# Kernel tuning notes

Hardware: AMD Instinct MI355X
Metric: run time of the kernel (lower is better)

The kernel has to match this reference:

```python
import jax, jax.numpy as jnp
import numpy as np

H = 16      # num_heads
EPS = 1e-6  # LayerNorm eps


def _ln(x, g, b):
    m = jnp.mean(x, -1, keepdims=True)
    v = jnp.mean((x - m) ** 2, -1, keepdims=True)
    return (x - m) / jnp.sqrt(v + EPS) * g + b


def _mha(q_in, k_in, v_in, qw, qb, kw, kb, vw, vb, pw, pb, mask):
    # q_in: (B, Sq, C); k_in/v_in: (B, Skv, C); mask: bool (Sq, Skv) or None (True = masked)
    B, Sq, C = q_in.shape
    hd = C // H

    def split(x, w, bb):
        return (x @ w + bb).reshape(B, -1, H, hd).transpose(0, 2, 1, 3)  # (B,H,S,hd)

    q = split(q_in, qw, qb) * hd ** -0.5
    k = split(k_in, kw, kb)
    v = split(v_in, vw, vb)
    s = jnp.einsum('bhqd,bhkd->bhqk', q, k)  # (B,H,Sq,Skv)
    if mask is not None:
        s = jnp.where(mask, -jnp.inf, s)
    a = jax.nn.softmax(s, axis=-1)
    o = jnp.einsum('bhqk,bhkd->bhqd', a, v)
    return o.transpose(0, 2, 1, 3).reshape(B, Sq, C) @ pw + pb


def _mlp(x, w1, b1, w2, b2):
    # torch nn.GELU default is exact (erf) gelu
    return jax.nn.gelu(x @ w1 + b1, approximate=False) @ w2 + b2


def setup_inputs() -> dict:
    key = jax.random.key(0)
    B, S, C, M = 1, 2048, 1024, 4096
    ks = iter(jax.random.split(key, 64))

    def w(shape):
        return jax.random.normal(next(ks), shape, jnp.float32) * 0.02

    inp = {
        'features': jax.random.normal(next(ks), (B, S, C), jnp.float32),
        'encoder_output': jax.random.normal(next(ks), (B, S, C), jnp.float32),
    }
    for p in ['ln1a', 'ln1b', 'ln2a', 'ln2b']:
        inp[p + '_g'] = jnp.ones((C,), jnp.float32)
        inp[p + '_b'] = jnp.zeros((C,), jnp.float32)
    for p in ['sa', 'ca']:
        for q in ['q', 'k', 'v', 'p']:
            inp[f'{p}_{q}w'] = w((C, C))
            inp[f'{p}_{q}b'] = jnp.zeros((C,), jnp.float32)
    for p in ['m1', 'm2']:
        inp[p + '_w1'] = w((C, M))
        inp[p + '_b1'] = jnp.zeros((M,), jnp.float32)
        inp[p + '_w2'] = w((M, C))
        inp[p + '_b2'] = jnp.zeros((C,), jnp.float32)
    return inp


def reference(features, encoder_output,
              ln1a_g, ln1a_b, ln1b_g, ln1b_b, ln2a_g, ln2a_b, ln2b_g, ln2b_b,
              sa_qw, sa_qb, sa_kw, sa_kb, sa_vw, sa_vb, sa_pw, sa_pb,
              ca_qw, ca_qb, ca_kw, ca_kb, ca_vw, ca_vb, ca_pw, ca_pb,
              m1_w1, m1_b1, m1_w2, m1_b2, m2_w1, m2_b1, m2_w2, m2_b2):
    S = features.shape[1]
    causal = jnp.triu(jnp.ones((S, S), dtype=bool), 1)  # look-ahead mask (decoder)
    # self-attention block (pre-norm, residual; dropout/drop-path identity in eval)
    xn = _ln(features, ln1a_g, ln1a_b)
    x = features + _mha(xn, xn, xn, sa_qw, sa_qb, sa_kw, sa_kb, sa_vw, sa_vb, sa_pw, sa_pb, causal)
    x = x + _mlp(_ln(x, ln1b_g, ln1b_b), m1_w1, m1_b1, m1_w2, m1_b2)
    # cross-attention block: k = v = encoder_output, q = norm(x)
    xn = _ln(x, ln2a_g, ln2a_b)
    x = x + _mha(xn, encoder_output, encoder_output, ca_qw, ca_qb, ca_kw, ca_kb, ca_vw, ca_vb, ca_pw, ca_pb, None)
    return x + _mlp(_ln(x, ln2b_g, ln2b_b), m2_w1, m2_b1, m2_w2, m2_b2)
```

## Files before the change

kernel.cpp:

```cpp
#include <hip/hip_runtime.h>
#include <math.h>

typedef unsigned short u16;
typedef __bf16 bf16_t;
typedef bf16_t bf16x8 __attribute__((ext_vector_type(8)));
typedef float f32x4 __attribute__((ext_vector_type(4)));
typedef float f32x16 __attribute__((ext_vector_type(16)));

#define DI __device__ __forceinline__

DI u16 f2bf(float f) {
  union { float f; unsigned u; } c; c.f = f;
  unsigned r = c.u + 0x7FFFu + ((c.u >> 16) & 1u);
  return (u16)(r >> 16);
}

DI unsigned pack2(float lo, float hi_) {
  return (unsigned)f2bf(lo) | ((unsigned)f2bf(hi_) << 16);
}

DI unsigned cvt_pk(float lo, float hi_) {
  unsigned d;
  asm("v_cvt_pk_bf16_f32 %0, %1, %2" : "=v"(d) : "v"(lo), "v"(hi_));
  return d;
}

typedef __attribute__((address_space(1))) void* gas_ptr;
typedef __attribute__((address_space(3))) void* las_ptr;

DI void gload16(const void* g, void* l) {
  __builtin_amdgcn_global_load_lds((gas_ptr)g, (las_ptr)l, 16, 0, 0);
}

struct TransArgs { const float* src[12]; u16* dst[12]; };
__global__ __launch_bounds__(256) void k_transpose_all(TransArgs ta) {
  __shared__ float tile[32][33];
  int bx = blockIdx.x;
  int z, local, K, N;
  if (bx < 8192) { z = bx >> 10; local = bx & 1023; K = 1024; N = 1024; }
  else {
    int i = bx - 8192; z = 8 + (i >> 12); local = i & 4095;
    if (z & 1) { K = 4096; N = 1024; } else { K = 1024; N = 4096; }
  }
  const float* w = ta.src[z];
  u16* wt = ta.dst[z];
  int nT = N >> 5;
  int n0 = (local % nT) * 32, k0 = (local / nT) * 32;
  int tx = threadIdx.x & 31, ty = threadIdx.x >> 5;
  for (int r = ty; r < 32; r += 8)
    tile[r][tx] = w[(size_t)(k0 + r) * N + n0 + tx];
  __syncthreads();
  for (int r = ty; r < 32; r += 8)
    wt[(size_t)(n0 + r) * K + k0 + tx] = f2bf(tile[tx][r]);
}

__global__ __launch_bounds__(256) void k_cvt(const float* __restrict__ in, u16* __restrict__ out, int n4) {
  int i = blockIdx.x * 256 + threadIdx.x;
  if (i < n4) {
    float4 v = ((const float4*)in)[i];
    ushort4 o;
    o.x = f2bf(v.x); o.y = f2bf(v.y); o.z = f2bf(v.z); o.w = f2bf(v.w);
    ((ushort4*)out)[i] = o;
  }
}

__global__ __launch_bounds__(256) void k_biaspack(float* __restrict__ bq, float* __restrict__ bc,
                                                  const float* qb, const float* kb, const float* vb,
                                                  const float* ckb, const float* cvb) {
  int i = blockIdx.x * 256 + threadIdx.x;
  if (i < 1024) bq[i] = qb[i];
  else if (i < 2048) bq[i] = kb[i - 1024];
  else if (i < 3072) bq[i] = vb[i - 2048];
  else if (i < 4096) bc[i - 3072] = ckb[i - 3072];
  else if (i < 5120) bc[i - 3072] = cvb[i - 4096];
}

__global__ __launch_bounds__(256) void k_ln(const float* __restrict__ x, const float* __restrict__ g,
                                            const float* __restrict__ b, u16* __restrict__ out) {
  int row = blockIdx.x, t = threadIdx.x;
  const float4 v = ((const float4*)(x + (size_t)row * 1024))[t];
  float s = v.x + v.y + v.z + v.w;
  float ss = v.x * v.x + v.y * v.y + v.z * v.z + v.w * v.w;
  for (int o = 32; o; o >>= 1) { s += __shfl_down(s, o); ss += __shfl_down(ss, o); }
  __shared__ float red[10];
  int w = t >> 6;
  if ((t & 63) == 0) { red[w] = s; red[4 + w] = ss; }
  __syncthreads();
  if (t == 0) {
    float S = red[0] + red[1] + red[2] + red[3];
    float SS = red[4] + red[5] + red[6] + red[7];
    float mean = S * (1.f / 1024.f);
    float var = SS * (1.f / 1024.f) - mean * mean;
    red[8] = mean; red[9] = rsqrtf(var + 1e-6f);
  }
  __syncthreads();
  float mean = red[8], rstd = red[9];
  float4 gg = ((const float4*)g)[t], bb = ((const float4*)b)[t];
  ushort4 o4;
  o4.x = f2bf((v.x - mean) * rstd * gg.x + bb.x);
  o4.y = f2bf((v.y - mean) * rstd * gg.y + bb.y);
  o4.z = f2bf((v.z - mean) * rstd * gg.z + bb.z);
  o4.w = f2bf((v.w - mean) * rstd * gg.w + bb.w);
  ((ushort4*)(out + (size_t)row * 1024))[t] = o4;
}

template <int MODE>
__global__ __launch_bounds__(256) void k_gemm(const u16* __restrict__ A, const u16* __restrict__ Bt,
                                              const float* __restrict__ bias, void* outv, u16* vtout,
                                              int M, int N, int K, int ostride,
                                              float scale, int scale_end, int vcol0) {
  constexpr int BM = 64, NT = 2;
  __shared__ u16 aL[2][BM * 64];
  __shared__ u16 bL[2][128 * 64];
  const int lane = threadIdx.x & 63, w = threadIdx.x >> 6, t = threadIdx.x;
  const int wn = w;
  const int m0 = blockIdx.y * BM, n0 = blockIdx.x * 128;

  f32x4 acc[4][NT];
#pragma unroll
  for (int i = 0; i < 4; ++i)
#pragma unroll
    for (int j = 0; j < NT; ++j) acc[i][j] = (f32x4){0.f, 0.f, 0.f, 0.f};

  auto stage = [&](int buf, int kt) {
    const int k0 = kt << 6;
#pragma unroll
    for (int c = t; c < BM * 8; c += 256) {
      int row = c >> 3, c16 = c & 7;
      int sw = (c16 * 16) ^ ((row & 7) << 4);
      gload16((const char*)(A + (size_t)(m0 + row) * K + k0) + sw, (char*)aL[buf] + c * 16);
    }
#pragma unroll
    for (int c = t; c < 1024; c += 256) {
      int row = c >> 3, c16 = c & 7;
      int sw = (c16 * 16) ^ ((row & 7) << 4);
      gload16((const char*)(Bt + (size_t)(n0 + row) * K + k0) + sw, (char*)bL[buf] + c * 16);
    }
  };

  const int nkt = K >> 6;
  stage(0, 0);
  __syncthreads();
  int cur = 0;
  for (int kt = 0; kt < nkt; ++kt) {
    if (kt + 1 < nkt) stage(cur ^ 1, kt + 1);
#pragma unroll
    for (int kk = 0; kk < 2; ++kk) {
      const int cb = kk * 64 + ((lane >> 4) << 4);
      bf16x8 af[4], bfr[NT];
#pragma unroll
      for (int mi = 0; mi < 4; ++mi) {
        int row = mi * 16 + (lane & 15);
        af[mi] = *(const bf16x8*)((const char*)aL[cur] + row * 128 + (cb ^ ((row & 7) << 4)));
      }
#pragma unroll
      for (int ni = 0; ni < NT; ++ni) {
        int row = wn * 32 + ni * 16 + (lane & 15);
        bfr[ni] = *(const bf16x8*)((const char*)bL[cur] + row * 128 + (cb ^ ((row & 7) << 4)));
      }
#pragma unroll
      for (int mi = 0; mi < 4; ++mi)
#pragma unroll
        for (int ni = 0; ni < NT; ++ni)
          acc[mi][ni] = __builtin_amdgcn_mfma_f32_16x16x32_bf16(af[mi], bfr[ni], acc[mi][ni], 0, 0, 0);
    }
    __syncthreads();
    cur ^= 1;
  }

  const int cBase = n0 + wn * 32 + (lane & 15);
  const int rBase = m0 + ((lane >> 4) << 2);
#pragma unroll
  for (int ni = 0; ni < NT; ++ni) {
    int col = cBase + ni * 16;
    float bv = bias[col];
#pragma unroll
    for (int mi = 0; mi < 4; ++mi) {
      int row = rBase + mi * 16;
      f32x4 a = acc[mi][ni];
      if (MODE == 0) {
        float sc = (col < scale_end) ? scale : 1.f;
        if (col >= vcol0) {
          ushort4 o4;
          o4.x = f2bf((a[0] + bv) * sc); o4.y = f2bf((a[1] + bv) * sc);
          o4.z = f2bf((a[2] + bv) * sc); o4.w = f2bf((a[3] + bv) * sc);
          *(ushort4*)(vtout + (size_t)(col - vcol0) * M + row) = o4;
        } else {
#pragma unroll
          for (int r = 0; r < 4; ++r)
            ((u16*)outv)[(size_t)(row + r) * ostride + col] = f2bf((a[r] + bv) * sc);
        }
      } else {
#pragma unroll
        for (int r = 0; r < 4; ++r) {
          float v = a[r] + bv;
          ((u16*)outv)[(size_t)(row + r) * ostride + col] =
              f2bf(0.5f * v * (1.f + erff(v * 0.70710678118654752f)));
        }
      }
    }
  }
}

template <int MODE>
__global__ __launch_bounds__(512, 2) void k_gemm_sk(const u16* __restrict__ A, const u16* __restrict__ Bt,
                                                    const float* __restrict__ bias, const float* res,
                                                    void* outv, int M, int N, int K, float scale) {
  __shared__ u16 aL[2][2][64 * 64];
  __shared__ u16 bL[2][2][64 * 64];
  const int t = threadIdx.x, lane = t & 63, w = t >> 6;
  const int kh = w >> 2, ws2 = w & 3;
  const int ts = t & 255;
  const int m0 = blockIdx.y * 64, n0 = blockIdx.x * 64;
  const int nktH = (K >> 6) >> 1;
  const int kbase = kh * nktH;

  f32x4 acc[4];
#pragma unroll
  for (int i = 0; i < 4; ++i) acc[i] = (f32x4){0.f, 0.f, 0.f, 0.f};

  auto stage = [&](int buf, int kt) {
    const int k0 = (kbase + kt) << 6;
#pragma unroll
    for (int i = 0; i < 2; ++i) {
      int c = i * 256 + ts;
      int row = c >> 3, c16 = c & 7;
      int sw = (c16 * 16) ^ ((row & 7) << 4);
      gload16((const char*)(A + (size_t)(m0 + row) * K + k0) + sw, (char*)aL[kh][buf] + c * 16);
      gload16((const char*)(Bt + (size_t)(n0 + row) * K + k0) + sw, (char*)bL[kh][buf] + c * 16);
    }
  };

  stage(0, 0);
  __syncthreads();
  int cur = 0;
  for (int kt = 0; kt < nktH; ++kt) {
    if (kt + 1 < nktH) stage(cur ^ 1, kt + 1);
#pragma unroll
    for (int kk = 0; kk < 2; ++kk) {
      const int cb = kk * 64 + ((lane >> 4) << 4);
      bf16x8 af[4], bfr;
#pragma unroll
      for (int mi = 0; mi < 4; ++mi) {
        int row = mi * 16 + (lane & 15);
        af[mi] = *(const bf16x8*)((const char*)aL[kh][cur] + row * 128 + (cb ^ ((row & 7) << 4)));
      }
      {
        int row = ws2 * 16 + (lane & 15);
        bfr = *(const bf16x8*)((const char*)bL[kh][cur] + row * 128 + (cb ^ ((row & 7) << 4)));
      }
#pragma unroll
      for (int mi = 0; mi < 4; ++mi)
        acc[mi] = __builtin_amdgcn_mfma_f32_16x16x32_bf16(af[mi], bfr, acc[mi], 0, 0, 0);
    }
    __syncthreads();
    cur ^= 1;
  }

  float* mergeF = (float*)aL;
  const int r0l = (lane >> 4) << 2, col16 = lane & 15;
  if (kh == 1) {
#pragma unroll
    for (int mi = 0; mi < 4; ++mi)
#pragma unroll
      for (int r = 0; r < 4; ++r)
        mergeF[(ws2 * 64 + mi * 16 + r0l + r) * 17 + col16] = acc[mi][r];
  }
  __syncthreads();
  if (kh == 0) {
    int col = n0 + ws2 * 16 + col16;
    float bv = bias[col];
#pragma unroll
    for (int mi = 0; mi < 4; ++mi) {
      int row = m0 + mi * 16 + r0l;
#pragma unroll
      for (int r = 0; r < 4; ++r) {
        float v = acc[mi][r] + mergeF[(ws2 * 64 + mi * 16 + r0l + r) * 17 + col16] + bv;
        size_t idx = (size_t)(row + r) * N + col;
        if (MODE == 0) ((u16*)outv)[idx] = f2bf(v * scale);
        else ((float*)outv)[idx] = res[idx] + v;
      }
    }
  }
}

template <bool CAUSAL>
__global__ __launch_bounds__(512, 2) void k_attn3(const u16* __restrict__ Q, const u16* __restrict__ K,
                                                  const u16* __restrict__ VT, u16* __restrict__ O,
                                                  int S, int qstride, int kstride) {
  __shared__ __align__(16) char smem[64 * 1024 + 2048 + 8192];
  const int t = threadIdx.x, lane = t & 63, w = t >> 6;
  const int ks = w & 3, qw = w >> 2;
  const int lo5 = lane & 31, hi = lane >> 5;
  const int h = blockIdx.x;
  const int bq = blockIdx.y;
  const int qt = (bq & 1) ? (31 - (bq >> 1)) : (bq >> 1);
  const int hd0 = h * 64;
  const int q0 = qt * 64 + qw * 32;
  const int ts = qw * 64 + lane;

  u16* kL = (u16*)(smem + ks * 16384);
  u16* vL = (u16*)(smem + ks * 16384 + 8192);

  auto issueK = [&](int kt) {
#pragma unroll
    for (int j = 0; j < 4; ++j) {
      int c = j * 128 + ts, row = c >> 3, c16 = c & 7;
      int sw = (c16 * 16) ^ ((row & 7) << 4);
      gload16((const char*)(K + (size_t)(kt * 64 + row) * kstride + hd0) + sw, (char*)kL + c * 16);
    }
  };
  auto issueV = [&](int kt) {
#pragma unroll
    for (int j = 0; j < 4; ++j) {
      int c = j * 128 + ts, row = c >> 3, c16 = c & 7;
      int sw = (c16 * 16) ^ ((row & 7) << 4);
      gload16((const char*)(VT + (size_t)(hd0 + row) * S + kt * 64) + sw, (char*)vL + c * 16);
    }
  };

  bf16x8 qf[4];
#pragma unroll
  for (int sl = 0; sl < 4; ++sl)
    qf[sl] = *(const bf16x8*)(Q + (size_t)(q0 + lo5) * qstride + hd0 + sl * 16 + hi * 8);

  f32x16 oa0 = {}, oa1 = {};
  float mrun = -1e30f, lsum = 0.f;

  const int nkt = CAUSAL ? (qt + 1) : (S >> 6);
  const int nIter = (nkt + 3) >> 2;

  if (ks < nkt) { issueK(ks); issueV(ks); }
  __syncthreads();

  for (int i = 0; i < nIter; ++i) {
    const int kt = ks + 4 * i;
    const bool active = kt < nkt;
    const bool nxt = kt + 4 < nkt;
    f32x16 s0 = {}, s1 = {};
    if (active) {
#pragma unroll
      for (int sl = 0; sl < 4; ++sl) {
        int cb = sl * 32 + hi * 16;
        int r0 = lo5, r1 = 32 + lo5;
        bf16x8 kf0 = *(const bf16x8*)((const char*)kL + r0 * 128 + (cb ^ ((r0 & 7) << 4)));
        bf16x8 kf1 = *(const bf16x8*)((const char*)kL + r1 * 128 + (cb ^ ((r1 & 7) << 4)));
        s0 = __builtin_amdgcn_mfma_f32_32x32x16_bf16(kf0, qf[sl], s0, 0, 0, 0);
        s1 = __builtin_amdgcn_mfma_f32_32x32x16_bf16(kf1, qf[sl], s1, 0, 0, 0);
      }
      if (CAUSAL && kt == qt) {
        int qg = q0 + lo5;
#pragma unroll
        for (int r = 0; r < 16; ++r) {
          int kg = kt * 64 + (r & 3) + 8 * (r >> 2) + 4 * hi;
          if (kg > qg) s0[r] = -1e30f;
          if (kg + 32 > qg) s1[r] = -1e30f;
        }
      }
      float mx[16];
#pragma unroll
      for (int r = 0; r < 16; ++r) mx[r] = fmaxf(s0[r], s1[r]);
#pragma unroll
      for (int st = 8; st; st >>= 1)
#pragma unroll
        for (int r = 0; r < 8; ++r)
          if (r < st) mx[r] = fmaxf(mx[r], mx[r + st]);
      float pm = fmaxf(mx[0], __shfl_xor(mx[0], 32));

      if (!__all(pm - mrun <= 8.f)) {
        float mnew = fmaxf(mrun, pm);
        float sc = exp2f(mrun - mnew);
        lsum *= sc;
#pragma unroll
        for (int r = 0; r < 16; ++r) { oa0[r] *= sc; oa1[r] *= sc; }
        mrun = mnew;
      }

#pragma unroll
      for (int r = 0; r < 16; ++r) s0[r] = exp2f(s0[r] - mrun);
#pragma unroll
      for (int r = 0; r < 16; ++r) s1[r] = exp2f(s1[r] - mrun);
      float sm[16];
#pragma unroll
      for (int r = 0; r < 16; ++r) sm[r] = s0[r] + s1[r];
#pragma unroll
      for (int st = 8; st; st >>= 1)
#pragma unroll
        for (int r = 0; r < 8; ++r)
          if (r < st) sm[r] += sm[r + st];
      lsum += sm[0] + __shfl_xor(sm[0], 32);
    }
    __syncthreads();
    if (nxt) issueK(kt + 4);
    if (active) {
#pragma unroll
      for (int ksl = 0; ksl < 4; ++ksl) {
        const int base = 8 * (ksl & 1);
        float pA0, pA1, pA2, pA3, pB0, pB1, pB2, pB3;
        if (ksl < 2) {
          pA0 = s0[base + 0]; pA1 = s0[base + 1]; pA2 = s0[base + 2]; pA3 = s0[base + 3];
          pB0 = s0[base + 4]; pB1 = s0[base + 5]; pB2 = s0[base + 6]; pB3 = s0[base + 7];
        } else {
          pA0 = s1[base + 0]; pA1 = s1[base + 1]; pA2 = s1[base + 2]; pA3 = s1[base + 3];
          pB0 = s1[base + 4]; pB1 = s1[base + 5]; pB2 = s1[base + 6]; pB3 = s1[base + 7];
        }
        unsigned a01 = cvt_pk(pA0, pA1), a23 = cvt_pk(pA2, pA3);
        unsigned b01 = cvt_pk(pB0, pB1), b23 = cvt_pk(pB2, pB3);
        unsigned xa01 = __shfl_xor(a01, 32), xa23 = __shfl_xor(a23, 32);
        unsigned xb01 = __shfl_xor(b01, 32), xb23 = __shfl_xor(b23, 32);
        union { unsigned u[4]; bf16x8 v; } pf;
        pf.u[0] = hi ? xb01 : a01;
        pf.u[1] = hi ? xb23 : a23;
        pf.u[2] = hi ? b01 : xa01;
        pf.u[3] = hi ? b23 : xa23;
        int cb = ksl * 32 + hi * 16;
        int r0 = lo5, r1 = 32 + lo5;
        bf16x8 vf0 = *(const bf16x8*)((const char*)vL + r0 * 128 + (cb ^ ((r0 & 7) << 4)));
        bf16x8 vf1 = *(const bf16x8*)((const char*)vL + r1 * 128 + (cb ^ ((r1 & 7) << 4)));
        oa0 = __builtin_amdgcn_mfma_f32_32x32x16_bf16(vf0, pf.v, oa0, 0, 0, 0);
        oa1 = __builtin_amdgcn_mfma_f32_32x32x16_bf16(vf1, pf.v, oa1, 0, 0, 0);
      }
    }
    __syncthreads();
    if (nxt) issueV(kt + 4);
  }
  __syncthreads();

  float* mlBuf = (float*)(smem + 65536);
#define OB_BYTE(g, halfoff) (lo5 * 256 + (((halfoff) + 32 * (g) + 16 * hi) ^ ((lo5 & 15) << 4)))
  if (ks >= 2) {
    char* ob = smem + (qw * 2 + (ks - 2)) * 8192;
#pragma unroll
    for (int g = 0; g < 4; ++g) {
      *(float4*)(ob + OB_BYTE(g, 0)) = make_float4(oa0[4 * g + 0], oa0[4 * g + 1], oa0[4 * g + 2], oa0[4 * g + 3]);
      *(float4*)(ob + OB_BYTE(g, 128)) = make_float4(oa1[4 * g + 0], oa1[4 * g + 1], oa1[4 * g + 2], oa1[4 * g + 3]);
    }
    if (hi == 0) { mlBuf[(w * 32 + lo5) * 2] = mrun; mlBuf[(w * 32 + lo5) * 2 + 1] = lsum; }
  }
  __syncthreads();
  if (ks < 2) {
    int pw = qw * 4 + ks + 2;
    char* ob = smem + (qw * 2 + ks) * 8192;
    float mB = mlBuf[(pw * 32 + lo5) * 2], lB = mlBuf[(pw * 32 + lo5) * 2 + 1];
    float M = fmaxf(mrun, mB);
    float sA = exp2f(mrun - M), sB = exp2f(mB - M);
    lsum = lsum * sA + lB * sB;
    mrun = M;
#pragma unroll
    for (int g = 0; g < 4; ++g) {
      float4 v0 = *(const float4*)(ob + OB_BYTE(g, 0));
      float4 v1 = *(const float4*)(ob + OB_BYTE(g, 128));
      oa0[4 * g + 0] = oa0[4 * g + 0] * sA + v0.x * sB;
      oa0[4 * g + 1] = oa0[4 * g + 1] * sA + v0.y * sB;
      oa0[4 * g + 2] = oa0[4 * g + 2] * sA + v0.z * sB;
      oa0[4 * g + 3] = oa0[4 * g + 3] * sA + v0.w * sB;
      oa1[4 * g + 0] = oa1[4 * g + 0] * sA + v1.x * sB;
      oa1[4 * g + 1] = oa1[4 * g + 1] * sA + v1.y * sB;
      oa1[4 * g + 2] = oa1[4 * g + 2] * sA + v1.z * sB;
      oa1[4 * g + 3] = oa1[4 * g + 3] * sA + v1.w * sB;
    }
  }
  if (ks == 1) {
    char* ob = smem + 32768 + qw * 8192;
#pragma unroll
    for (int g = 0; g < 4; ++g) {
      *(float4*)(ob + OB_BYTE(g, 0)) = make_float4(oa0[4 * g + 0], oa0[4 * g + 1], oa0[4 * g + 2], oa0[4 * g + 3]);
      *(float4*)(ob + OB_BYTE(g, 128)) = make_float4(oa1[4 * g + 0], oa1[4 * g + 1], oa1[4 * g + 2], oa1[4 * g + 3]);
    }
    if (hi == 0) { mlBuf[(w * 32 + lo5) * 2] = mrun; mlBuf[(w * 32 + lo5) * 2 + 1] = lsum; }
  }
  __syncthreads();
  if (ks == 0) {
    int pw = qw * 4 + 1;
    char* ob = smem + 32768 + qw * 8192;
    float mB = mlBuf[(pw * 32 + lo5) * 2], lB = mlBuf[(pw * 32 + lo5) * 2 + 1];
    float M = fmaxf(mrun, mB);
    float sA = exp2f(mrun - M), sB = exp2f(mB - M);
    lsum = lsum * sA + lB * sB;
#pragma unroll
    for (int g = 0; g < 4; ++g) {
      float4 v0 = *(const float4*)(ob + OB_BYTE(g, 0));
      float4 v1 = *(const float4*)(ob + OB_BYTE(g, 128));
      oa0[4 * g + 0] = oa0[4 * g + 0] * sA + v0.x * sB;
      oa0[4 * g + 1] = oa0[4 * g + 1] * sA + v0.y * sB;
      oa0[4 * g + 2] = oa0[4 * g + 2] * sA + v0.z * sB;
      oa0[4 * g + 3] = oa0[4 * g + 3] * sA + v0.w * sB;
      oa1[4 * g + 0] = oa1[4 * g + 0] * sA + v1.x * sB;
      oa1[4 * g + 1] = oa1[4 * g + 1] * sA + v1.y * sB;
      oa1[4 * g + 2] = oa1[4 * g + 2] * sA + v1.z * sB;
      oa1[4 * g + 3] = oa1[4 * g + 3] * sA + v1.w * sB;
    }
    float inv = 1.f / lsum;
    u16* ldsO = (u16*)(smem + 65536 + 2048);
    int qrow = qw * 32 + lo5;
#pragma unroll
    for (int g = 0; g < 4; ++g) {
      unsigned w0 = cvt_pk(oa0[4 * g + 0] * inv, oa0[4 * g + 1] * inv);
      unsigned w1 = cvt_pk(oa0[4 * g + 2] * inv, oa0[4 * g + 3] * inv);
      int dby = (8 * g + 4 * hi) * 2;
      *(uint2*)((char*)ldsO + qrow * 128 + (dby ^ ((qrow & 7) << 4))) = make_uint2(w0, w1);
      unsigned w2 = cvt_pk(oa1[4 * g + 0] * inv, oa1[4 * g + 1] * inv);
      unsigned w3 = cvt_pk(oa1[4 * g + 2] * inv, oa1[4 * g + 3] * inv);
      int dby2 = (32 + 8 * g + 4 * hi) * 2;
      *(uint2*)((char*)ldsO + qrow * 128 + (dby2 ^ ((qrow & 7) << 4))) = make_uint2(w2, w3);
    }
  }
  __syncthreads();
  {
    u16* ldsO = (u16*)(smem + 65536 + 2048);
    int c = t, row = c >> 3, c16 = c & 7;
    uint4 val = *(const uint4*)((const char*)ldsO + row * 128 + ((c16 * 16) ^ ((row & 7) << 4)));
    *(uint4*)(O + (size_t)(qt * 64 + row) * 1024 + hd0 + c16 * 8) = val;
  }
#undef OB_BYTE
}

extern "C" void kernel_launch(void* const* d_in, const int* in_sizes, int n_in,
                              void* d_out, int out_size, void* d_ws, size_t ws_size,
                              hipStream_t stream) {
  const float* features = (const float*)d_in[0];
  const float* enc      = (const float*)d_in[1];
  const float* g1a = (const float*)d_in[2];  const float* b1a = (const float*)d_in[3];
  const float* g1b = (const float*)d_in[4];  const float* b1b = (const float*)d_in[5];
  const float* g2a = (const float*)d_in[6];  const float* b2a = (const float*)d_in[7];
  const float* g2b = (const float*)d_in[8];  const float* b2b = (const float*)d_in[9];
  const float* sa_qw = (const float*)d_in[10]; const float* sa_qb = (const float*)d_in[11];
  const float* sa_kw = (const float*)d_in[12]; const float* sa_kb = (const float*)d_in[13];
  const float* sa_vw = (const float*)d_in[14]; const float* sa_vb = (const float*)d_in[15];
  const float* sa_pw = (const float*)d_in[16]; const float* sa_pb = (const float*)d_in[17];
  const float* ca_qw = (const float*)d_in[18]; const float* ca_qb = (const float*)d_in[19];
  const float* ca_kw = (const float*)d_in[20]; const float* ca_kb = (const float*)d_in[21];
  const float* ca_vw = (const float*)d_in[22]; const float* ca_vb = (const float*)d_in[23];
  const float* ca_pw = (const float*)d_in[24]; const float* ca_pb = (const float*)d_in[25];
  const float* m1_w1 = (const float*)d_in[26]; const float* m1_b1 = (const float*)d_in[27];
  const float* m1_w2 = (const float*)d_in[28]; const float* m1_b2 = (const float*)d_in[29];
  const float* m2_w1 = (const float*)d_in[30]; const float* m2_b1 = (const float*)d_in[31];
  const float* m2_w2 = (const float*)d_in[32]; const float* m2_b2 = (const float*)d_in[33];

  const int S = 2048, C = 1024, Mh = 4096;
  const size_t CC = (size_t)C * C;
  float* xout = (float*)d_out;

  char* p = (char*)d_ws;
  auto take = [&](size_t bytes) { char* q = p; p += (bytes + 255) & ~(size_t)255; return q; };
  u16* wt_qkv  = (u16*)take(3 * CC * 2);
  u16* wt_sap  = (u16*)take(CC * 2);
  u16* wt_cap  = (u16*)take(CC * 2);
  u16* wt_caq  = (u16*)take(CC * 2);
  u16* wt_ckv  = (u16*)take(2 * CC * 2);
  u16* wt_m1w1 = (u16*)take((size_t)C * Mh * 2);
  u16* wt_m1w2 = (u16*)take((size_t)C * Mh * 2);
  u16* wt_m2w1 = (u16*)take((size_t)C * Mh * 2);
  u16* wt_m2w2 = (u16*)take((size_t)C * Mh * 2);
  float* bias_qkv = (float*)take(3 * C * 4);
  float* bias_ckv = (float*)take(2 * C * 4);
  u16* xn   = (u16*)take((size_t)S * C * 2);
  u16* encb = (u16*)take((size_t)S * C * 2);
  u16* vtbuf = (u16*)take((size_t)C * S * 2);
  u16* abuf  = (u16*)take((size_t)S * C * 2);
  u16* hbuf  = (u16*)take((size_t)S * Mh * 2);
  u16* qkbuf = hbuf;
  u16* qbuf  = hbuf + (size_t)4 * 1024 * 1024;
  u16* kvbuf = hbuf + (size_t)6 * 1024 * 1024;

  dim3 blk(256);
  const float qs2 = 0.125f * 1.4426950408889634f;
  const int BIG = 1 << 30;

  TransArgs ta;
  ta.src[0] = sa_qw;  ta.dst[0] = wt_qkv;
  ta.src[1] = sa_kw;  ta.dst[1] = wt_qkv + CC;
  ta.src[2] = sa_vw;  ta.dst[2] = wt_qkv + 2 * CC;
  ta.src[3] = sa_pw;  ta.dst[3] = wt_sap;
  ta.src[4] = ca_pw;  ta.dst[4] = wt_cap;
  ta.src[5] = ca_qw;  ta.dst[5] = wt_caq;
  ta.src[6] = ca_kw;  ta.dst[6] = wt_ckv;
  ta.src[7] = ca_vw;  ta.dst[7] = wt_ckv + CC;
  ta.src[8] = m1_w1;  ta.dst[8] = wt_m1w1;
  ta.src[9] = m1_w2;  ta.dst[9] = wt_m1w2;
  ta.src[10] = m2_w1; ta.dst[10] = wt_m2w1;
  ta.src[11] = m2_w2; ta.dst[11] = wt_m2w2;
  k_transpose_all<<<dim3(8192 + 16384), blk, 0, stream>>>(ta);
  k_cvt<<<dim3(S * C / 1024), blk, 0, stream>>>(enc, encb, S * C / 4);
  k_biaspack<<<20, blk, 0, stream>>>(bias_qkv, bias_ckv, sa_qb, sa_kb, sa_vb, ca_kb, ca_vb);

  k_ln<<<S, blk, 0, stream>>>(features, g1a, b1a, xn);
  k_gemm<0><<<dim3(24, 32), blk, 0, stream>>>(xn, wt_qkv, bias_qkv, qkbuf, vtbuf,
                                              S, 3072, C, 2048, qs2, 1024, 2048);
  k_attn3<true><<<dim3(16, 32), dim3(512), 0, stream>>>(qkbuf, qkbuf + 1024, vtbuf, abuf, S, 2048, 2048);
  k_gemm_sk<1><<<dim3(16, 32), dim3(512), 0, stream>>>(abuf, wt_sap, sa_pb, features, xout, S, C, C, 1.f);
  k_ln<<<S, blk, 0, stream>>>(xout, g1b, b1b, xn);
  k_gemm<2><<<dim3(32, 32), blk, 0, stream>>>(xn, wt_m1w1, m1_b1, hbuf, nullptr,
                                              S, Mh, C, Mh, 1.f, 0, BIG);
  k_gemm_sk<1><<<dim3(16, 32), dim3(512), 0, stream>>>(hbuf, wt_m1w2, m1_b2, xout, xout, S, C, Mh, 1.f);
  k_ln<<<S, blk, 0, stream>>>(xout, g2a, b2a, xn);
  k_gemm_sk<0><<<dim3(16, 32), dim3(512), 0, stream>>>(xn, wt_caq, ca_qb, nullptr, qbuf, S, C, C, qs2);
  k_gemm<0><<<dim3(16, 32), blk, 0, stream>>>(encb, wt_ckv, bias_ckv, kvbuf, vtbuf,
                                              S, 2048, C, 1024, 1.f, 0, 1024);
  k_attn3<false><<<dim3(16, 32), dim3(512), 0, stream>>>(qbuf, kvbuf, vtbuf, abuf, S, 1024, 1024);
  k_gemm_sk<1><<<dim3(16, 32), dim3(512), 0, stream>>>(abuf, wt_cap, ca_pb, xout, xout, S, C, C, 1.f);
  k_ln<<<S, blk, 0, stream>>>(xout, g2b, b2b, xn);
  k_gemm<2><<<dim3(32, 32), blk, 0, stream>>>(xn, wt_m2w1, m2_b1, hbuf, nullptr,
                                              S, Mh, C, Mh, 1.f, 0, BIG);
  k_gemm_sk<1><<<dim3(16, 32), dim3(512), 0, stream>>>(hbuf, wt_m2w2, m2_b2, xout, xout, S, C, Mh, 1.f);
}
```

Measured before the change: 360.4 us.

## Load attention K/V fragments directly from global memory, dropping LDS staging

The attention kernel no longer stages K and V tiles through LDS with async global-to-LDS loads and barriers. Each wave now reads its MFMA operand fragments straight from global memory (relying on L2/L1), which removes the per-iteration syncthreads and the staging code. LDS shrinks to the epilogue merge buffers, and launch bounds rise to 4 blocks per CU for more occupancy. The cost is no data sharing across the two query waves that used the same K/V tile, more global traffic, and exposed load latency without explicit prefetch.

```diff
diff --git a/kernel.cpp b/kernel.cpp
--- a/kernel.cpp
+++ b/kernel.cpp
@@ -13,10 +13,6 @@
   union { float f; unsigned u; } c; c.f = f;
   unsigned r = c.u + 0x7FFFu + ((c.u >> 16) & 1u);
   return (u16)(r >> 16);
-}
-
-DI unsigned pack2(float lo, float hi_) {
-  return (unsigned)f2bf(lo) | ((unsigned)f2bf(hi_) << 16);
 }
 
 DI unsigned cvt_pk(float lo, float hi_) {
@@ -285,10 +281,10 @@
 }
 
 template <bool CAUSAL>
-__global__ __launch_bounds__(512, 2) void k_attn3(const u16* __restrict__ Q, const u16* __restrict__ K,
+__global__ __launch_bounds__(512, 4) void k_attn4(const u16* __restrict__ Q, const u16* __restrict__ K,
                                                   const u16* __restrict__ VT, u16* __restrict__ O,
                                                   int S, int qstride, int kstride) {
-  __shared__ __align__(16) char smem[64 * 1024 + 2048 + 8192];
+  __shared__ __align__(16) char smem[48 * 1024 + 2048 + 8192];
   const int t = threadIdx.x, lane = t & 63, w = t >> 6;
   const int ks = w & 3, qw = w >> 2;
   const int lo5 = lane & 31, hi = lane >> 5;
@@ -297,27 +293,6 @@
   const int qt = (bq & 1) ? (31 - (bq >> 1)) : (bq >> 1);
   const int hd0 = h * 64;
   const int q0 = qt * 64 + qw * 32;
-  const int ts = qw * 64 + lane;
-
-  u16* kL = (u16*)(smem + ks * 16384);
-  u16* vL = (u16*)(smem + ks * 16384 + 8192);
-
-  auto issueK = [&](int kt) {
-#pragma unroll
-    for (int j = 0; j < 4; ++j) {
-      int c = j * 128 + ts, row = c >> 3, c16 = c & 7;
-      int sw = (c16 * 16) ^ ((row & 7) << 4);
-      gload16((const char*)(K + (size_t)(kt * 64 + row) * kstride + hd0) + sw, (char*)kL + c * 16);
-    }
-  };
-  auto issueV = [&](int kt) {
-#pragma unroll
-    for (int j = 0; j < 4; ++j) {
-      int c = j * 128 + ts, row = c >> 3, c16 = c & 7;
-      int sw = (c16 * 16) ^ ((row & 7) << 4);
-      gload16((const char*)(VT + (size_t)(hd0 + row) * S + kt * 64) + sw, (char*)vL + c * 16);
-    }
-  };
 
   bf16x8 qf[4];
 #pragma unroll
@@ -328,105 +303,91 @@
   float mrun = -1e30f, lsum = 0.f;
 
   const int nkt = CAUSAL ? (qt + 1) : (S >> 6);
-  const int nIter = (nkt + 3) >> 2;
-
-  if (ks < nkt) { issueK(ks); issueV(ks); }
-  __syncthreads();
-
-  for (int i = 0; i < nIter; ++i) {
-    const int kt = ks + 4 * i;
-    const bool active = kt < nkt;
-    const bool nxt = kt + 4 < nkt;
+  const u16* Kb = K + (size_t)lo5 * kstride + hd0 + hi * 8;
+  const u16* Vb = VT + (size_t)(hd0 + lo5) * S + hi * 8;
+
+  for (int kt = ks; kt < nkt; kt += 4) {
+    const u16* Kt = Kb + (size_t)(kt * 64) * kstride;
     f32x16 s0 = {}, s1 = {};
-    if (active) {
-#pragma unroll
-      for (int sl = 0; sl < 4; ++sl) {
-        int cb = sl * 32 + hi * 16;
-        int r0 = lo5, r1 = 32 + lo5;
-        bf16x8 kf0 = *(const bf16x8*)((const char*)kL + r0 * 128 + (cb ^ ((r0 & 7) << 4)));
-        bf16x8 kf1 = *(const bf16x8*)((const char*)kL + r1 * 128 + (cb ^ ((r1 & 7) << 4)));
-        s0 = __builtin_amdgcn_mfma_f32_32x32x16_bf16(kf0, qf[sl], s0, 0, 0, 0);
-        s1 = __builtin_amdgcn_mfma_f32_32x32x16_bf16(kf1, qf[sl], s1, 0, 0, 0);
-      }
-      if (CAUSAL && kt == qt) {
-        int qg = q0 + lo5;
-#pragma unroll
-        for (int r = 0; r < 16; ++r) {
-          int kg = kt * 64 + (r & 3) + 8 * (r >> 2) + 4 * hi;
-          if (kg > qg) s0[r] = -1e30f;
-          if (kg + 32 > qg) s1[r] = -1e30f;
-        }
-      }
-      float mx[16];
-#pragma unroll
-      for (int r = 0; r < 16; ++r) mx[r] = fmaxf(s0[r], s1[r]);
-#pragma unroll
-      for (int st = 8; st; st >>= 1)
-#pragma unroll
-        for (int r = 0; r < 8; ++r)
-          if (r < st) mx[r] = fmaxf(mx[r], mx[r + st]);
-      float pm = fmaxf(mx[0], __shfl_xor(mx[0], 32));
-
-      if (!__all(pm - mrun <= 8.f)) {
-        float mnew = fmaxf(mrun, pm);
-        float sc = exp2f(mrun - mnew);
-        lsum *= sc;
-#pragma unroll
-        for (int r = 0; r < 16; ++r) { oa0[r] *= sc; oa1[r] *= sc; }
-        mrun = mnew;
-      }
-
-#pragma unroll
-      for (int r = 0; r < 16; ++r) s0[r] = exp2f(s0[r] - mrun);
-#pragma unroll
-      for (int r = 0; r < 16; ++r) s1[r] = exp2f(s1[r] - mrun);
-      float sm[16];
-#pragma unroll
-      for (int r = 0; r < 16; ++r) sm[r] = s0[r] + s1[r];
-#pragma unroll
-      for (int st = 8; st; st >>= 1)
-#pragma unroll
-        for (int r = 0; r < 8; ++r)
-          if (r < st) sm[r] += sm[r + st];
-      lsum += sm[0] + __shfl_xor(sm[0], 32);
-    }
-    __syncthreads();
-    if (nxt) issueK(kt + 4);
-    if (active) {
-#pragma unroll
-      for (int ksl = 0; ksl < 4; ++ksl) {
-        const int base = 8 * (ksl & 1);
-        float pA0, pA1, pA2, pA3, pB0, pB1, pB2, pB3;
-        if (ksl < 2) {
-          pA0 = s0[base + 0]; pA1 = s0[base + 1]; pA2 = s0[base + 2]; pA3 = s0[base + 3];
-          pB0 = s0[base + 4]; pB1 = s0[base + 5]; pB2 = s0[base + 6]; pB3 = s0[base + 7];
-        } else {
-          pA0 = s1[base + 0]; pA1 = s1[base + 1]; pA2 = s1[base + 2]; pA3 = s1[base + 3];
-          pB0 = s1[base + 4]; pB1 = s1[base + 5]; pB2 = s1[base + 6]; pB3 = s1[base + 7];
-        }
-        unsigned a01 = cvt_pk(pA0, pA1), a23 = cvt_pk(pA2, pA3);
-        unsigned b01 = cvt_pk(pB0, pB1), b23 = cvt_pk(pB2, pB3);
-        unsigned xa01 = __shfl_xor(a01, 32), xa23 = __shfl_xor(a23, 32);
-        unsigned xb01 = __shfl_xor(b01, 32), xb23 = __shfl_xor(b23, 32);
-        union { unsigned u[4]; bf16x8 v; } pf;
-        pf.u[0] = hi ? xb01 : a01;
-        pf.u[1] = hi ? xb23 : a23;
-        pf.u[2] = hi ? b01 : xa01;
-        pf.u[3] = hi ? b23 : xa23;
-        int cb = ksl * 32 + hi * 16;
-        int r0 = lo5, r1 = 32 + lo5;
-        bf16x8 vf0 = *(const bf16x8*)((const char*)vL + r0 * 128 + (cb ^ ((r0 & 7) << 4)));
-        bf16x8 vf1 = *(const bf16x8*)((const char*)vL + r1 * 128 + (cb ^ ((r1 & 7) << 4)));
-        oa0 = __builtin_amdgcn_mfma_f32_32x32x16_bf16(vf0, pf.v, oa0, 0, 0, 0);
-        oa1 = __builtin_amdgcn_mfma_f32_32x32x16_bf16(vf1, pf.v, oa1, 0, 0, 0);
-      }
-    }
-    __syncthreads();
-    if (nxt) issueV(kt + 4);
-  }
-  __syncthreads();
-
-  float* mlBuf = (float*)(smem + 65536);
+#pragma unroll
+    for (int sl = 0; sl < 4; ++sl) {
+      bf16x8 kf0 = *(const bf16x8*)(Kt + sl * 16);
+      bf16x8 kf1 = *(const bf16x8*)(Kt + (size_t)32 * kstride + sl * 16);
+      s0 = __builtin_amdgcn_mfma_f32_32x32x16_bf16(kf0, qf[sl], s0, 0, 0, 0);
+      s1 = __builtin_amdgcn_mfma_f32_32x32x16_bf16(kf1, qf[sl], s1, 0, 0, 0);
+    }
+    if (CAUSAL && kt == qt) {
+      int qg = q0 + lo5;
+#pragma unroll
+      for (int r = 0; r < 16; ++r) {
+        int kg = kt * 64 + (r & 3) + 8 * (r >> 2) + 4 * hi;
+        if (kg > qg) s0[r] = -1e30f;
+        if (kg + 32 > qg) s1[r] = -1e30f;
+      }
+    }
+    float mx[16];
+#pragma unroll
+    for (int r = 0; r < 16; ++r) mx[r] = fmaxf(s0[r], s1[r]);
+#pragma unroll
+    for (int st = 8; st; st >>= 1)
+#pragma unroll
+      for (int r = 0; r < 8; ++r)
+        if (r < st) mx[r] = fmaxf(mx[r], mx[r + st]);
+    float pm = fmaxf(mx[0], __shfl_xor(mx[0], 32));
+
+    if (!__all(pm - mrun <= 8.f)) {
+      float mnew = fmaxf(mrun, pm);
+      float sc = exp2f(mrun - mnew);
+      lsum *= sc;
+#pragma unroll
+      for (int r = 0; r < 16; ++r) { oa0[r] *= sc; oa1[r] *= sc; }
+      mrun = mnew;
+    }
+
+#pragma unroll
+    for (int r = 0; r < 16; ++r) s0[r] = exp2f(s0[r] - mrun);
+#pragma unroll
+    for (int r = 0; r < 16; ++r) s1[r] = exp2f(s1[r] - mrun);
+    float sm[16];
+#pragma unroll
+    for (int r = 0; r < 16; ++r) sm[r] = s0[r] + s1[r];
+#pragma unroll
+    for (int st = 8; st; st >>= 1)
+#pragma unroll
+      for (int r = 0; r < 8; ++r)
+        if (r < st) sm[r] += sm[r + st];
+    lsum += sm[0] + __shfl_xor(sm[0], 32);
+
+    const u16* Vt = Vb + kt * 64;
+#pragma unroll
+    for (int ksl = 0; ksl < 4; ++ksl) {
+      const int base = 8 * (ksl & 1);
+      float pA0, pA1, pA2, pA3, pB0, pB1, pB2, pB3;
+      if (ksl < 2) {
+        pA0 = s0[base + 0]; pA1 = s0[base + 1]; pA2 = s0[base + 2]; pA3 = s0[base + 3];
+        pB0 = s0[base + 4]; pB1 = s0[base + 5]; pB2 = s0[base + 6]; pB3 = s0[base + 7];
+      } else {
+        pA0 = s1[base + 0]; pA1 = s1[base + 1]; pA2 = s1[base + 2]; pA3 = s1[base + 3];
+        pB0 = s1[base + 4]; pB1 = s1[base + 5]; pB2 = s1[base + 6]; pB3 = s1[base + 7];
+      }
+      unsigned a01 = cvt_pk(pA0, pA1), a23 = cvt_pk(pA2, pA3);
+      unsigned b01 = cvt_pk(pB0, pB1), b23 = cvt_pk(pB2, pB3);
+      unsigned xa01 = __shfl_xor(a01, 32), xa23 = __shfl_xor(a23, 32);
+      unsigned xb01 = __shfl_xor(b01, 32), xb23 = __shfl_xor(b23, 32);
+      union { unsigned u[4]; bf16x8 v; } pf;
+      pf.u[0] = hi ? xb01 : a01;
+      pf.u[1] = hi ? xb23 : a23;
+      pf.u[2] = hi ? b01 : xa01;
+      pf.u[3] = hi ? b23 : xa23;
+      bf16x8 vf0 = *(const bf16x8*)(Vt + ksl * 16);
+      bf16x8 vf1 = *(const bf16x8*)(Vt + (size_t)32 * S + ksl * 16);
+      oa0 = __builtin_amdgcn_mfma_f32_32x32x16_bf16(vf0, pf.v, oa0, 0, 0, 0);
+      oa1 = __builtin_amdgcn_mfma_f32_32x32x16_bf16(vf1, pf.v, oa1, 0, 0, 0);
+    }
+  }
+  __syncthreads();
+
+  float* mlBuf = (float*)(smem + 49152);
 #define OB_BYTE(g, halfoff) (lo5 * 256 + (((halfoff) + 32 * (g) + 16 * hi) ^ ((lo5 & 15) << 4)))
   if (ks >= 2) {
     char* ob = smem + (qw * 2 + (ks - 2)) * 8192;
@@ -491,7 +452,7 @@
       oa1[4 * g + 3] = oa1[4 * g + 3] * sA + v1.w * sB;
     }
     float inv = 1.f / lsum;
-    u16* ldsO = (u16*)(smem + 65536 + 2048);
+    u16* ldsO = (u16*)(smem + 49152 + 2048);
     int qrow = qw * 32 + lo5;
 #pragma unroll
     for (int g = 0; g < 4; ++g) {
@@ -507,7 +468,7 @@
   }
   __syncthreads();
   {
-    u16* ldsO = (u16*)(smem + 65536 + 2048);
+    u16* ldsO = (u16*)(smem + 49152 + 2048);
     int c = t, row = c >> 3, c16 = c & 7;
     uint4 val = *(const uint4*)((const char*)ldsO + row * 128 + ((c16 * 16) ^ ((row & 7) << 4)));
     *(uint4*)(O + (size_t)(qt * 64 + row) * 1024 + hd0 + c16 * 8) = val;
@@ -587,7 +548,7 @@
   k_ln<<<S, blk, 0, stream>>>(features, g1a, b1a, xn);
   k_gemm<0><<<dim3(24, 32), blk, 0, stream>>>(xn, wt_qkv, bias_qkv, qkbuf, vtbuf,
                                               S, 3072, C, 2048, qs2, 1024, 2048);
-  k_attn3<true><<<dim3(16, 32), dim3(512), 0, stream>>>(qkbuf, qkbuf + 1024, vtbuf, abuf, S, 2048, 2048);
+  k_attn4<true><<<dim3(16, 32), dim3(512), 0, stream>>>(qkbuf, qkbuf + 1024, vtbuf, abuf, S, 2048, 2048);
   k_gemm_sk<1><<<dim3(16, 32), dim3(512), 0, stream>>>(abuf, wt_sap, sa_pb, features, xout, S, C, C, 1.f);
   k_ln<<<S, blk, 0, stream>>>(xout, g1b, b1b, xn);
   k_gemm<2><<<dim3(32, 32), blk, 0, stream>>>(xn, wt_m1w1, m1_b1, hbuf, nullptr,
@@ -597,7 +558,7 @@
   k_gemm_sk<0><<<dim3(16, 32), dim3(512), 0, stream>>>(xn, wt_caq, ca_qb, nullptr, qbuf, S, C, C, qs2);
   k_gemm<0><<<dim3(16, 32), blk, 0, stream>>>(encb, wt_ckv, bias_ckv, kvbuf, vtbuf,
                                               S, 2048, C, 1024, 1.f, 0, 1024);
-  k_attn3<false><<<dim3(16, 32), dim3(512), 0, stream>>>(qbuf, kvbuf, vtbuf, abuf, S, 1024, 1024);
+  k_attn4<false><<<dim3(16, 32), dim3(512), 0, stream>>>(qbuf, kvbuf, vtbuf, abuf, S, 1024, 1024);
   k_gemm_sk<1><<<dim3(16, 32), dim3(512), 0, stream>>>(abuf, wt_cap, ca_pb, xout, xout, S, C, C, 1.f);
   k_ln<<<S, blk, 0, stream>>>(xout, g2b, b2b, xn);
   k_gemm<2><<<dim3(32, 32), blk, 0, stream>>>(xn, wt_m2w1, m2_b1, hbuf, nullptr,
```

Measured after the change: 391.4 us. +8.6%, slower.
